# Kernel optimization log

Measured on AMD Instinct MI355X. Metric: run time of the kernel, lower is better.

## Reference

```python
import jax, jax.numpy as jnp
import numpy as np

GRID_SIZE, SPLINE_ORDER = 5, 3  # efficient-kan KANLinear defaults
NUM_BASES = GRID_SIZE + SPLINE_ORDER


def b_splines(x, grid):
    # x: (N, in_dim), grid: (in_dim, GRID_SIZE + 2*SPLINE_ORDER + 1)
    xe = x[..., None]
    bases = ((xe >= grid[:, :-1]) & (xe < grid[:, 1:])).astype(x.dtype)
    for k in range(1, SPLINE_ORDER + 1):  # Cox-de Boor recursion (static, 3 iters)
        left = (xe - grid[:, : -(k + 1)]) / (grid[:, k:-1] - grid[:, : -(k + 1)])
        right = (grid[:, k + 1:] - xe) / (grid[:, k + 1:] - grid[:, 1:-k])
        bases = left * bases[..., :-1] + right * bases[..., 1:]
    return bases  # (N, in_dim, NUM_BASES)


def kan_linear(x, grid, base_w, spline_w, scaler):
    # base branch: SiLU(x) @ W_base^T ; spline branch: B-spline basis @ scaled spline weights
    n = x.shape[0]
    out_dim = base_w.shape[0]
    base = jax.nn.silu(x) @ base_w.T
    bs = b_splines(x, grid).reshape(n, -1)                    # (N, in*NUM_BASES)
    sw = (spline_w * scaler[..., None]).reshape(out_dim, -1)  # (out, in*NUM_BASES)
    return base + bs @ sw.T


def setup_inputs() -> dict:
    key = jax.random.key(0)
    N, E, F, H, C, L = 50000, 500000, 128, 128, 40, 3
    ks = jax.random.split(key, 8)
    x = jax.random.normal(ks[0], (N, F), dtype=jnp.float32)
    edge_index = jax.random.randint(ks[1], (2, E), 0, N)
    # KAN grid (registered buffer in efficient-kan): uniform over [-1,1] extended by spline_order
    h_step = 2.0 / GRID_SIZE
    pts = np.arange(-SPLINE_ORDER, GRID_SIZE + SPLINE_ORDER + 1) * h_step - 1.0
    grid_mp = jnp.asarray(np.tile(pts, (F, 1)), dtype=jnp.float32)
    D = F + L * H  # skip-concat dim into output KANLinear
    grid_out = jnp.asarray(np.tile(pts, (D, 1)), dtype=jnp.float32)
    s = 0.1
    conv_base_w = jax.random.normal(ks[2], (L, H, F), dtype=jnp.float32) * s
    conv_spline_w = jax.random.normal(ks[3], (L, H, F, NUM_BASES), dtype=jnp.float32) * s
    conv_scaler = jnp.ones((L, H, F), dtype=jnp.float32)
    conv_bias = jnp.zeros((L, H), dtype=jnp.float32)
    bn_gamma = jnp.ones((L, H), dtype=jnp.float32)
    bn_beta = jnp.zeros((L, H), dtype=jnp.float32)
    out_base_w = jax.random.normal(ks[4], (C, D), dtype=jnp.float32) * s
    out_spline_w = jax.random.normal(ks[5], (C, D, NUM_BASES), dtype=jnp.float32) * s
    out_scaler = jnp.ones((C, D), dtype=jnp.float32)
    return dict(x=x, edge_index=edge_index, grid_mp=grid_mp, conv_base_w=conv_base_w,
                conv_spline_w=conv_spline_w, conv_scaler=conv_scaler, conv_bias=conv_bias,
                bn_gamma=bn_gamma, bn_beta=bn_beta, grid_out=grid_out,
                out_base_w=out_base_w, out_spline_w=out_spline_w, out_scaler=out_scaler)


def reference(x, edge_index, grid_mp, conv_base_w, conv_spline_w, conv_scaler, conv_bias,
              bn_gamma, bn_beta, grid_out, out_base_w, out_spline_w, out_scaler):
    N = x.shape[0]
    L = conv_base_w.shape[0]
    # GCN normalization with self-loops (computed once; identical each layer)
    loop = jnp.arange(N)
    src = jnp.concatenate([edge_index[0], loop])
    dst = jnp.concatenate([edge_index[1], loop])
    deg = jax.ops.segment_sum(jnp.ones_like(src, dtype=x.dtype), dst, num_segments=N)
    dinv = jnp.where(deg > 0, jax.lax.rsqrt(jnp.maximum(deg, 1.0)), 0.0)
    norm = dinv[src] * dinv[dst]  # (E+N,)
    feats = [x]
    for i in range(L):  # static layer loop
        h = kan_linear(x, grid_mp, conv_base_w[i], conv_spline_w[i], conv_scaler[i])
        # symmetric-normalized sparse aggregation (gather on src, scatter-add on dst)
        h = jax.ops.segment_sum(h[src] * norm[:, None], dst, num_segments=N) + conv_bias[i]
        # BatchNorm1d (training mode: biased batch statistics over nodes)
        mu = h.mean(axis=0)
        var = h.var(axis=0)
        x = (h - mu) * jax.lax.rsqrt(var + 1e-5) * bn_gamma[i] + bn_beta[i]
        feats.append(x)  # dropout p=0.0 is identity
    xc = jnp.concatenate(feats, axis=1)  # skip-concat: (N, F + L*H)
    logits = kan_linear(xc, grid_out, out_base_w, out_spline_w, out_scaler)
    return jax.nn.log_softmax(logits, axis=1)
```

## Files before the change

kernel.cpp:

```cpp
#include <hip/hip_runtime.h>
#include <hip/hip_bf16.h>
#include <math.h>

#define F_IN   128
#define HID    128
#define NLAYER 3
#define NCLS   40
#define DCAT   512
#define OOUT   64

typedef short s16x8 __attribute__((ext_vector_type(8)));
typedef unsigned short u16x8 __attribute__((ext_vector_type(8)));
typedef unsigned short u16x4 __attribute__((ext_vector_type(4)));
typedef float f32x4 __attribute__((ext_vector_type(4)));


static __device__ __forceinline__ float silu_f(float x) {
    return x / (1.f + __expf(-x));
}

static __device__ __forceinline__ unsigned short f2bf_rn(float f) {
    union { __hip_bfloat16 h; unsigned short u; } cv;
    cv.h = __float2bfloat16(f);
    return cv.u;
}

static __device__ __forceinline__ void gload_lds16(const void* g, void* l) {
    __builtin_amdgcn_global_load_lds(
        (const __attribute__((address_space(1))) void*)g,
        (__attribute__((address_space(3))) void*)l, 16, 0, 0);
}


__global__ __launch_bounds__(256) void deg_init_kernel(int* deg, int N) {
    for (int i = blockIdx.x * blockDim.x + threadIdx.x; i < N; i += gridDim.x * blockDim.x)
        deg[i] = 1;
}

__global__ __launch_bounds__(256) void deg_count_kernel(const int* __restrict__ dst, int E, int* deg) {
    for (int i = blockIdx.x * blockDim.x + threadIdx.x; i < E; i += gridDim.x * blockDim.x)
        atomicAdd(&deg[dst[i]], 1);
}

__global__ __launch_bounds__(256) void dinv_kernel(const int* __restrict__ deg, float* dinv, int N) {
    for (int i = blockIdx.x * blockDim.x + threadIdx.x; i < N; i += gridDim.x * blockDim.x)
        dinv[i] = rsqrtf((float)deg[i]);
}

__global__ __launch_bounds__(256) void scan_reduce_kernel(const int* __restrict__ deg, int* __restrict__ bsum, int N) {
    __shared__ int sh[256];
    int t = threadIdx.x;
    int e = blockIdx.x * 256 + t;
    sh[t] = (e < N) ? deg[e] : 0;
    __syncthreads();
#pragma unroll
    for (int off = 128; off > 0; off >>= 1) {
        if (t < off) sh[t] += sh[t + off];
        __syncthreads();
    }
    if (t == 0) bsum[blockIdx.x] = sh[0];
}

__global__ __launch_bounds__(256) void scan_top_kernel(const int* __restrict__ bsum, int* __restrict__ bbase, int nsb) {
    __shared__ int sh[256];
    int t = threadIdx.x;
    int chunk = (nsb + 255) >> 8;
    int begin = t * chunk;
    int end = begin + chunk; if (end > nsb) end = nsb;
    int s = 0;
    for (int i = begin; i < end; ++i) s += bsum[i];
    sh[t] = s;
    __syncthreads();
#pragma unroll
    for (int off = 1; off < 256; off <<= 1) {
        int v = 0;
        if (t >= off) v = sh[t - off];
        __syncthreads();
        if (t >= off) sh[t] += v;
        __syncthreads();
    }
    int run = (t == 0) ? 0 : sh[t - 1];
    for (int i = begin; i < end; ++i) {
        bbase[i] = run;
        run += bsum[i];
    }
}

__global__ __launch_bounds__(256) void scan_write_kernel(const int* __restrict__ deg,
                                                         const int* __restrict__ bbase,
                                                         int* __restrict__ offs, int* __restrict__ cursor, int N) {
    __shared__ int sh[256];
    int t = threadIdx.x;
    int e = blockIdx.x * 256 + t;
    int d = (e < N) ? deg[e] : 0;
    sh[t] = d;
    __syncthreads();
#pragma unroll
    for (int off = 1; off < 256; off <<= 1) {
        int v = 0;
        if (t >= off) v = sh[t - off];
        __syncthreads();
        if (t >= off) sh[t] += v;
        __syncthreads();
    }
    int incl = sh[t] + bbase[blockIdx.x];
    int excl = incl - d;
    if (e < N) {
        offs[e] = excl;
        cursor[e] = excl;
        if (e == N - 1) offs[N] = incl;
    }
}

__global__ __launch_bounds__(256) void fill_kernel(const int* __restrict__ src, const int* __restrict__ dst,
                                                   int E, int N, int* cursor, int* __restrict__ csr) {
    int total = E + N;
    for (int i = blockIdx.x * blockDim.x + threadIdx.x; i < total; i += gridDim.x * blockDim.x) {
        if (i < E) {
            int d = dst[i];
            int p = atomicAdd(&cursor[d], 1);
            csr[p] = src[i];
        } else {
            int n = i - E;
            int p = atomicAdd(&cursor[n], 1);
            csr[p] = n;
        }
    }
}

__global__ __launch_bounds__(256) void pack_conv_mfma(const float* __restrict__ bw,
                                                      const float* __restrict__ sw,
                                                      const float* __restrict__ sc,
                                                      unsigned short* __restrict__ wpk) {
    int total = NLAYER * 9 * 4 * 8 * 64 * 8;
    for (int idx = blockIdx.x * blockDim.x + threadIdx.x; idx < total; idx += gridDim.x * blockDim.x) {
        int e    = idx & 7;
        int lane = (idx >> 3) & 63;
        int cf   = (idx >> 9) & 7;
        int kk   = (idx >> 12) & 3;
        int cc   = (idx >> 14) % 9;
        int l    = idx / (9 << 14);
        int o = cf * 16 + (lane & 15);
        int k = kk * 32 + ((lane >> 4) << 3) + e;
        float v;
        if (cc == 8) {
            v = bw[(l * 128 + o) * 128 + k];
        } else {
            int f = cc * 16 + (k >> 3);
            int j = k & 7;
            int base = (l * 128 + o) * 128 + f;
            v = sw[base * 8 + j] * sc[base];
        }
        wpk[idx] = f2bf_rn(v);
    }
}

__global__ __launch_bounds__(256) void pack_out_mfma(const float* __restrict__ bw,
                                                     const float* __restrict__ sw,
                                                     const float* __restrict__ sc,
                                                     unsigned short* __restrict__ wpk) {
    int total = 36 * 4 * 4 * 64 * 8;
    for (int idx = blockIdx.x * blockDim.x + threadIdx.x; idx < total; idx += gridDim.x * blockDim.x) {
        int e    = idx & 7;
        int lane = (idx >> 3) & 63;
        int cf   = (idx >> 9) & 3;
        int kk   = (idx >> 11) & 3;
        int gcc  = idx >> 13;
        int g = gcc / 9, cc = gcc % 9;
        int o = cf * 16 + (lane & 15);
        int k = kk * 32 + ((lane >> 4) << 3) + e;
        float v = 0.f;
        if (o < NCLS) {
            if (cc == 8) {
                int f = g * 128 + k;
                v = bw[o * DCAT + f];
            } else {
                int f = g * 128 + cc * 16 + (k >> 3);
                int j = k & 7;
                int base = o * DCAT + f;
                v = sw[base * 8 + j] * sc[base];
            }
        }
        wpk[idx] = f2bf_rn(v);
    }
}


__global__ __launch_bounds__(256) void copyx_kernel(const float* __restrict__ x, float* __restrict__ xc, int N) {
    int total = N * F_IN;
    for (int idx = blockIdx.x * blockDim.x + threadIdx.x; idx < total; idx += gridDim.x * blockDim.x) {
        int n = idx >> 7, f = idx & 127;
        xc[(size_t)n * DCAT + f] = x[idx];
    }
}

__global__ __launch_bounds__(512) void affine_init_kernel(float* scA, float* shA) {
    int i = threadIdx.x;
    scA[i] = 1.f; shA[i] = 0.f;
}

template<bool CONV, bool INIT>
__global__ __launch_bounds__(256, 2) void kan_fused_kernel(
    const float* __restrict__ xc, int in_off,
    const float* __restrict__ scA, const float* __restrict__ shA,
    const unsigned short* __restrict__ wconv,
    const unsigned short* __restrict__ wout,
    unsigned short* __restrict__ silbuf,
    unsigned short* __restrict__ htmp,
    const float* __restrict__ dinv,
    float* __restrict__ out_acc, int N) {

    __shared__ __align__(16) char lds_phi0[16384];
    __shared__ __align__(16) char lds_phi1[16384];

    const int tid = threadIdx.x;
    const int lane = tid & 63;
    const int wave = tid >> 6;
    const int l15 = lane & 15, lg = lane >> 4;
    const int nblk = blockIdx.x * 64;

    const float g0 = -1.f - 3.f * 0.4f;
    const float invh = 1.f / 0.4f;

    const int fg = tid & 3;
    const int n0 = tid >> 2;

    f32x4 accc[4][2];
    f32x4 acco[4];
    if (CONV) {
#pragma unroll
        for (int r = 0; r < 4; ++r)
#pragma unroll
            for (int c = 0; c < 2; ++c) accc[r][c] = (f32x4)0.f;
    }
#pragma unroll
    for (int r = 0; r < 4; ++r) acco[r] = (f32x4)0.f;

    float4 xqb[2], scb[2], shb[2];
    auto ldx = [&](int cc, int slot) {
        int f0 = in_off + cc * 16 + fg * 4;
        scb[slot] = *(const float4*)(scA + f0);
        shb[slot] = *(const float4*)(shA + f0);
        int gn = nblk + n0;
        xqb[slot] = (gn < N) ? *(const float4*)(xc + (size_t)gn * DCAT + f0) : (float4){0.f,0.f,0.f,0.f};
    };

    s16x8 wc_reg[4][2];
    s16x8 wo_reg[4];
    auto loadW = [&](int cc) {
        if (CONV) {
            const unsigned short* wcb = wconv + (size_t)cc * 16384;
#pragma unroll
            for (int kk = 0; kk < 4; ++kk)
#pragma unroll
                for (int c = 0; c < 2; ++c) {
                    int cf = wave * 2 + c;
                    wc_reg[kk][c] = *(const s16x8*)(wcb + (((size_t)kk * 8 + cf) * 64 + lane) * 8);
                }
        }
        const unsigned short* wob = wout + (size_t)cc * 8192;
#pragma unroll
        for (int kk = 0; kk < 4; ++kk)
            wo_reg[kk] = *(const s16x8*)(wob + (((size_t)kk * 4 + wave) * 64 + lane) * 8);
    };

    u16x8 pcur[4];
    auto phi_compute = [&](int ccc, int slot) {
        float xi[4] = {xqb[slot].x, xqb[slot].y, xqb[slot].z, xqb[slot].w};
        float scr[4] = {scb[slot].x, scb[slot].y, scb[slot].z, scb[slot].w};
        float shr[4] = {shb[slot].x, shb[slot].y, shb[slot].z, shb[slot].w};
        u16x4 sv;
#pragma unroll
        for (int fl = 0; fl < 4; ++fl) {
            float y = fmaf(xi[fl], scr[fl], shr[fl]);
            sv[fl] = f2bf_rn(silu_f(y));
            float t = (y - g0) * invh;
            float cf = floorf(t);
            int c = (int)cf;
            float u = t - cf;
            float um = 1.f - u;
            float u2 = u * u;
            float um2 = um * um;
            float w0 = um2 * um * (1.f / 6.f);
            float w3 = u2 * u * (1.f / 6.f);
            float w1 = fmaf(fmaf(0.5f, u, -1.f), u2, 2.f / 3.f);
            float w2 = fmaf(fmaf(-0.5f, u, 0.5f), u2, fmaf(0.5f, u, 1.f / 6.f));
            bool e[11];
#pragma unroll
            for (int v = 0; v < 11; ++v) e[v] = (c == v);
#pragma unroll
            for (int s = 0; s < 8; ++s) {
                float val = 0.f;
                val = e[s] ? w3 : val;
                val = e[s + 1] ? w2 : val;
                val = e[s + 2] ? w1 : val;
                val = e[s + 3] ? w0 : val;
                pcur[fl][s] = f2bf_rn(val);
            }
        }
        int gn = nblk + n0;
        if (gn < N) {
            int fdst = (ccc * 16 + fg * 4) ^ ((n0 & 7) << 3);
            *(u16x4*)(silbuf + (size_t)gn * 128 + fdst) = sv;
        }
    };

    auto write_phi = [&](char* buf) {
        int swz = (n0 & 7) << 4;
#pragma unroll
        for (int i = 0; i < 4; ++i) {
            int byte = n0 * 256 + ((fg * 64 + i * 16) ^ swz);
            *(u16x8*)(buf + byte) = pcur[i];
        }
    };

    auto mfma_phase = [&](const char* buf) {
#pragma unroll
        for (int kk = 0; kk < 4; ++kk) {
            const int kb = kk * 64 + lg * 16;
            s16x8 af[4];
#pragma unroll
            for (int r = 0; r < 4; ++r) {
                int n = r * 16 + l15;
                af[r] = *(const s16x8*)(buf + n * 256 + (kb ^ ((n & 7) << 4)));
            }
            if (CONV) {
#pragma unroll
                for (int c = 0; c < 2; ++c)
#pragma unroll
                    for (int r = 0; r < 4; ++r)
                        accc[r][c] = __builtin_amdgcn_mfma_f32_16x16x32_bf16(af[r], wc_reg[kk][c], accc[r][c], 0, 0, 0);
            }
#pragma unroll
            for (int r = 0; r < 4; ++r)
                acco[r] = __builtin_amdgcn_mfma_f32_16x16x32_bf16(af[r], wo_reg[kk], acco[r], 0, 0, 0);
        }
    };

    ldx(0, 0);
    phi_compute(0, 0);
    ldx(1, 1);
    loadW(0);
    write_phi(lds_phi0);
    __syncthreads();

#pragma unroll
    for (int cc = 0; cc < 9; ++cc) {
        char* cur = (cc & 1) ? lds_phi1 : lds_phi0;
        char* nxt = (cc & 1) ? lds_phi0 : lds_phi1;
        mfma_phase(cur);
        if (cc < 8) loadW(cc + 1);
        if (cc < 7) {
            ldx(cc + 2, cc & 1);
            phi_compute(cc + 1, (cc + 1) & 1);
            write_phi(nxt);
        }
        if (cc == 7) {
            const unsigned short* ssrc = silbuf + (size_t)nblk * 128;
#pragma unroll
            for (int i = 0; i < 4; ++i) {
                int e = tid + i * 256;
                gload_lds16(ssrc + e * 8, nxt + e * 16);
            }
        }
        if (cc < 8) __syncthreads();
    }

#pragma unroll
    for (int r = 0; r < 4; ++r) {
        int nb = nblk + r * 16 + lg * 4;
        if (CONV) {
#pragma unroll
            for (int c = 0; c < 2; ++c) {
                int o = wave * 32 + c * 16 + l15;
#pragma unroll
                for (int q = 0; q < 4; ++q) {
                    int n = nb + q;
                    if (n < N) htmp[(size_t)n * HID + o] = f2bf_rn(accc[r][c][q] * dinv[n]);
                }
            }
        }
        {
            int o = wave * 16 + l15;
            if (o < NCLS) {
#pragma unroll
                for (int q = 0; q < 4; ++q) {
                    int n = nb + q;
                    if (n < N) {
                        size_t a = (size_t)n * OOUT + o;
                        float v = acco[r][q];
                        if (!INIT) v += out_acc[a];
                        out_acc[a] = v;
                    }
                }
            }
        }
    }
}

__global__ __launch_bounds__(256) void agg_kernel(const unsigned short* __restrict__ h,
                                                  const float* __restrict__ dinv,
                                                  const int* __restrict__ offs,
                                                  const int* __restrict__ csr,
                                                  const float* __restrict__ bias,
                                                  float* __restrict__ xc, int out_off, int N) {
    int n = blockIdx.x * 4 + (threadIdx.x >> 6);
    if (n >= N) return;
    int lane = threadIdx.x & 63;
    int s = offs[n], e = offs[n + 1];
    float a0 = 0.f, a1 = 0.f, b0 = 0.f, b1 = 0.f;
    float c0 = 0.f, c1 = 0.f, d0 = 0.f, d1 = 0.f;
    int i = s;
    for (; i + 4 <= e; i += 4) {
        int v0 = csr[i], v1 = csr[i + 1], v2 = csr[i + 2], v3 = csr[i + 3];
        unsigned u0 = *(const unsigned*)(h + (size_t)v0 * HID + lane * 2);
        unsigned u1 = *(const unsigned*)(h + (size_t)v1 * HID + lane * 2);
        unsigned u2 = *(const unsigned*)(h + (size_t)v2 * HID + lane * 2);
        unsigned u3 = *(const unsigned*)(h + (size_t)v3 * HID + lane * 2);
        a0 += __uint_as_float(u0 << 16);
        a1 += __uint_as_float(u0 & 0xffff0000u);
        b0 += __uint_as_float(u1 << 16);
        b1 += __uint_as_float(u1 & 0xffff0000u);
        c0 += __uint_as_float(u2 << 16);
        c1 += __uint_as_float(u2 & 0xffff0000u);
        d0 += __uint_as_float(u3 << 16);
        d1 += __uint_as_float(u3 & 0xffff0000u);
    }
    for (; i < e; ++i) {
        int v = csr[i];
        unsigned u = *(const unsigned*)(h + (size_t)v * HID + lane * 2);
        a0 += __uint_as_float(u << 16);
        a1 += __uint_as_float(u & 0xffff0000u);
    }
    a0 += b0 + c0 + d0;
    a1 += b1 + c1 + d1;
    float dn = dinv[n];
    float2 bv = *(const float2*)(bias + lane * 2);
    float2 res = {fmaf(a0, dn, bv.x), fmaf(a1, dn, bv.y)};
    *(float2*)(xc + (size_t)n * DCAT + out_off + lane * 2) = res;
}

__global__ __launch_bounds__(128) void bn_stats_kernel(const float* __restrict__ xc, int off, int N,
                                                       float* __restrict__ bnsum, float* __restrict__ bnsq) {
    int f = threadIdx.x;
    float s = 0.f, q = 0.f;
    for (int n = blockIdx.x; n < N; n += gridDim.x) {
        float v = xc[(size_t)n * DCAT + off + f];
        s += v;
        q += v * v;
    }
    atomicAdd(&bnsum[f], s);
    atomicAdd(&bnsq[f], q);
}

__global__ __launch_bounds__(128) void bn_affine_kernel(const float* __restrict__ bnsum,
                                                        const float* __restrict__ bnsq,
                                                        const float* __restrict__ gamma,
                                                        const float* __restrict__ beta,
                                                        float* scA, float* shA, int seg_off, float invN) {
    int f = threadIdx.x;
    float mu = bnsum[f] * invN;
    float var = bnsq[f] * invN - mu * mu;
    float rs = rsqrtf(var + 1e-5f);
    float s = gamma[f] * rs;
    scA[seg_off + f] = s;
    shA[seg_off + f] = fmaf(-mu, s, beta[f]);
}

__global__ __launch_bounds__(256) void logsoftmax_kernel(const float* __restrict__ oacc,
                                                         float* __restrict__ out, int N) {
    for (int n = blockIdx.x * blockDim.x + threadIdx.x; n < N; n += gridDim.x * blockDim.x) {
        const float* row = oacc + (size_t)n * OOUT;
        float m = -1e30f;
#pragma unroll
        for (int j = 0; j < NCLS; ++j) m = fmaxf(m, row[j]);
        float s = 0.f;
#pragma unroll
        for (int j = 0; j < NCLS; ++j) s += __expf(row[j] - m);
        float lse = m + __logf(s);
        float* orow = out + (size_t)n * NCLS;
#pragma unroll
        for (int j = 0; j < NCLS; ++j) orow[j] = row[j] - lse;
    }
}


extern "C" void kernel_launch(void* const* d_in, const int* in_sizes, int n_in,
                              void* d_out, int out_size, void* d_ws, size_t ws_size,
                              hipStream_t stream) {
    const float* x            = (const float*)d_in[0];
    const int*   eidx         = (const int*)d_in[1];
    const float* conv_base_w  = (const float*)d_in[3];
    const float* conv_spline_w= (const float*)d_in[4];
    const float* conv_scaler  = (const float*)d_in[5];
    const float* conv_bias    = (const float*)d_in[6];
    const float* bn_gamma     = (const float*)d_in[7];
    const float* bn_beta      = (const float*)d_in[8];
    const float* out_base_w   = (const float*)d_in[10];
    const float* out_spline_w = (const float*)d_in[11];
    const float* out_scaler   = (const float*)d_in[12];
    float* out = (float*)d_out;

    int N = in_sizes[0] / F_IN;
    int E = in_sizes[1] / 2;
    const int* esrc = eidx;
    const int* edst = eidx + E;

    int blocks = (N + 63) / 64;
    int npad = blocks * 64;
    int nsb = (N + 255) / 256;

    char* p = (char*)d_ws;
    auto carve = [&](size_t bytes) {
        char* r = p;
        p += (bytes + 255) & ~(size_t)255;
        return r;
    };
    float* xc   = (float*)carve((size_t)N * DCAT * 4);
    unsigned short* htmp = (unsigned short*)carve((size_t)npad * HID * 2);
    float* oacc = (float*)carve((size_t)npad * OOUT * 4);
    unsigned short* silbuf = (unsigned short*)carve((size_t)npad * 128 * 2);
    float* dinv = (float*)carve((size_t)N * 4);
    float* bn   = (float*)carve((size_t)NLAYER * 2 * HID * 4);
    float* scA  = (float*)carve((size_t)DCAT * 4);
    float* shA  = (float*)carve((size_t)DCAT * 4);
    unsigned short* wpkc = (unsigned short*)carve((size_t)NLAYER * 9 * 128 * 128 * 2);
    unsigned short* wpko = (unsigned short*)carve((size_t)36 * 64 * 128 * 2);
    int* deg    = (int*)carve((size_t)N * 4);
    int* offs   = (int*)carve((size_t)(N + 1) * 4);
    int* cursor = (int*)carve((size_t)(N + 1) * 4);
    int* bsum   = (int*)carve((size_t)nsb * 4);
    int* bbase  = (int*)carve((size_t)nsb * 4);
    int* csr    = (int*)carve((size_t)(E + N) * 4);

    hipMemsetAsync(bn, 0, NLAYER * 2 * HID * 4, stream);

    deg_init_kernel<<<512, 256, 0, stream>>>(deg, N);
    deg_count_kernel<<<1024, 256, 0, stream>>>(edst, E, deg);
    dinv_kernel<<<512, 256, 0, stream>>>(deg, dinv, N);
    scan_reduce_kernel<<<nsb, 256, 0, stream>>>(deg, bsum, N);
    scan_top_kernel<<<1, 256, 0, stream>>>(bsum, bbase, nsb);
    scan_write_kernel<<<nsb, 256, 0, stream>>>(deg, bbase, offs, cursor, N);
    fill_kernel<<<1024, 256, 0, stream>>>(esrc, edst, E, N, cursor, csr);

    pack_conv_mfma<<<1024, 256, 0, stream>>>(conv_base_w, conv_spline_w, conv_scaler, wpkc);
    pack_out_mfma<<<1024, 256, 0, stream>>>(out_base_w, out_spline_w, out_scaler, wpko);
    copyx_kernel<<<2048, 256, 0, stream>>>(x, xc, N);
    affine_init_kernel<<<1, 512, 0, stream>>>(scA, shA);

    float invN = 1.f / (float)N;
    for (int l = 0; l < NLAYER; ++l) {
        int in_off = l * HID;
        int out_off = (l + 1) * HID;
        const unsigned short* wl = wpkc + (size_t)l * 9 * 16384;
        const unsigned short* wo = wpko + (size_t)l * 9 * 8192;
        if (l == 0)
            kan_fused_kernel<true, true><<<blocks, 256, 0, stream>>>(
                xc, in_off, scA, shA, wl, wo, silbuf, htmp, dinv, oacc, N);
        else
            kan_fused_kernel<true, false><<<blocks, 256, 0, stream>>>(
                xc, in_off, scA, shA, wl, wo, silbuf, htmp, dinv, oacc, N);
        agg_kernel<<<(N + 3) / 4, 256, 0, stream>>>(htmp, dinv, offs, csr, conv_bias + l * HID, xc, out_off, N);
        float* bnsum = bn + l * 2 * HID;
        float* bnsq  = bnsum + HID;
        bn_stats_kernel<<<256, 128, 0, stream>>>(xc, out_off, N, bnsum, bnsq);
        bn_affine_kernel<<<1, 128, 0, stream>>>(bnsum, bnsq, bn_gamma + l * HID, bn_beta + l * HID,
                                                scA, shA, out_off, invN);
    }

    kan_fused_kernel<false, false><<<blocks, 256, 0, stream>>>(
        xc, 384, scA, shA, nullptr, wpko + (size_t)3 * 9 * 8192, silbuf, nullptr, dinv, oacc, N);

    logsoftmax_kernel<<<(N + 255) / 256, 256, 0, stream>>>(oacc, out, N);
}
```

Measured before the change: 545.5 us.

## Keep SiLU features in registers instead of a global scratch round-trip

The fused KAN kernel no longer writes SiLU-activated bf16 features to a global scratch buffer and reloads them into LDS via global_load_lds. It keeps them in registers across the chunk loop and writes them straight into the LDS tile in the last phase. The x prefetch is hoisted ahead of the MFMA phase, and __syncthreads is replaced by an explicit lgkmcnt wait plus s_barrier. This removes global traffic and a dependent load, but holds eight more u16x4 registers per thread, which may add register pressure under launch_bounds(256,2). The last kernel call now passes htmp where nullptr was passed before, though that branch does not use it.

```diff
diff --git a/kernel.cpp b/kernel.cpp
--- a/kernel.cpp
+++ b/kernel.cpp
@@ -25,10 +25,9 @@
     return cv.u;
 }
 
-static __device__ __forceinline__ void gload_lds16(const void* g, void* l) {
-    __builtin_amdgcn_global_load_lds(
-        (const __attribute__((address_space(1))) void*)g,
-        (__attribute__((address_space(3))) void*)l, 16, 0, 0);
+static __device__ __forceinline__ void lds_barrier() {
+    asm volatile("s_waitcnt lgkmcnt(0)" ::: "memory");
+    __builtin_amdgcn_s_barrier();
 }
 
 
@@ -205,7 +204,6 @@
     const float* __restrict__ scA, const float* __restrict__ shA,
     const unsigned short* __restrict__ wconv,
     const unsigned short* __restrict__ wout,
-    unsigned short* __restrict__ silbuf,
     unsigned short* __restrict__ htmp,
     const float* __restrict__ dinv,
     float* __restrict__ out_acc, int N) {
@@ -263,6 +261,8 @@
         for (int kk = 0; kk < 4; ++kk)
             wo_reg[kk] = *(const s16x8*)(wob + (((size_t)kk * 4 + wave) * 64 + lane) * 8);
     };
+
+    u16x4 sreg[8];
 
     u16x8 pcur[4];
     auto phi_compute = [&](int ccc, int slot) {
@@ -298,11 +298,7 @@
                 pcur[fl][s] = f2bf_rn(val);
             }
         }
-        int gn = nblk + n0;
-        if (gn < N) {
-            int fdst = (ccc * 16 + fg * 4) ^ ((n0 & 7) << 3);
-            *(u16x4*)(silbuf + (size_t)gn * 128 + fdst) = sv;
-        }
+        sreg[ccc] = sv;
     };
 
     auto write_phi = [&](char* buf) {
@@ -311,6 +307,15 @@
         for (int i = 0; i < 4; ++i) {
             int byte = n0 * 256 + ((fg * 64 + i * 16) ^ swz);
             *(u16x8*)(buf + byte) = pcur[i];
+        }
+    };
+
+    auto write_silu = [&](char* buf) {
+        int swz = (n0 & 7) << 4;
+#pragma unroll
+        for (int ccc = 0; ccc < 8; ++ccc) {
+            int byte = n0 * 256 + (((ccc * 16 + fg * 4) * 2) ^ swz);
+            *(u16x4*)(buf + byte) = sreg[ccc];
         }
     };
 
@@ -348,22 +353,15 @@
     for (int cc = 0; cc < 9; ++cc) {
         char* cur = (cc & 1) ? lds_phi1 : lds_phi0;
         char* nxt = (cc & 1) ? lds_phi0 : lds_phi1;
+        if (cc < 7) ldx(cc + 2, cc & 1);
         mfma_phase(cur);
         if (cc < 8) loadW(cc + 1);
         if (cc < 7) {
-            ldx(cc + 2, cc & 1);
             phi_compute(cc + 1, (cc + 1) & 1);
             write_phi(nxt);
         }
-        if (cc == 7) {
-            const unsigned short* ssrc = silbuf + (size_t)nblk * 128;
-#pragma unroll
-            for (int i = 0; i < 4; ++i) {
-                int e = tid + i * 256;
-                gload_lds16(ssrc + e * 8, nxt + e * 16);
-            }
-        }
-        if (cc < 8) __syncthreads();
+        if (cc == 7) write_silu(nxt);
+        if (cc < 8) lds_barrier();
     }
 
 #pragma unroll
@@ -519,7 +517,6 @@
     float* xc   = (float*)carve((size_t)N * DCAT * 4);
     unsigned short* htmp = (unsigned short*)carve((size_t)npad * HID * 2);
     float* oacc = (float*)carve((size_t)npad * OOUT * 4);
-    unsigned short* silbuf = (unsigned short*)carve((size_t)npad * 128 * 2);
     float* dinv = (float*)carve((size_t)N * 4);
     float* bn   = (float*)carve((size_t)NLAYER * 2 * HID * 4);
     float* scA  = (float*)carve((size_t)DCAT * 4);
@@ -556,10 +553,10 @@
         const unsigned short* wo = wpko + (size_t)l * 9 * 8192;
         if (l == 0)
             kan_fused_kernel<true, true><<<blocks, 256, 0, stream>>>(
-                xc, in_off, scA, shA, wl, wo, silbuf, htmp, dinv, oacc, N);
+                xc, in_off, scA, shA, wl, wo, htmp, dinv, oacc, N);
         else
             kan_fused_kernel<true, false><<<blocks, 256, 0, stream>>>(
-                xc, in_off, scA, shA, wl, wo, silbuf, htmp, dinv, oacc, N);
+                xc, in_off, scA, shA, wl, wo, htmp, dinv, oacc, N);
         agg_kernel<<<(N + 3) / 4, 256, 0, stream>>>(htmp, dinv, offs, csr, conv_bias + l * HID, xc, out_off, N);
         float* bnsum = bn + l * 2 * HID;
         float* bnsq  = bnsum + HID;
@@ -569,7 +566,7 @@
     }
 
     kan_fused_kernel<false, false><<<blocks, 256, 0, stream>>>(
-        xc, 384, scA, shA, nullptr, wpko + (size_t)3 * 9 * 8192, silbuf, nullptr, dinv, oacc, N);
+        xc, 384, scA, shA, nullptr, wpko + (size_t)3 * 9 * 8192, htmp, dinv, oacc, N);
 
     logsoftmax_kernel<<<(N + 255) / 256, 256, 0, stream>>>(oacc, out, N);
 }
```

Result: no change. 537.3 us (-1.5%).
